# Optimization experiments

Hardware: AMD Instinct MI355X
Metric: run time of the kernel (lower is better)

The kernel has to match this reference:

```python
import jax, jax.numpy as jnp
import numpy as np

B, S, D = 8, 2048, 768
SCALE = jnp.sqrt(jnp.float32(D))


def setup_inputs() -> dict:
    key = jax.random.key(0)
    ks = jax.random.split(key, 9)
    sd = 1.0 / np.sqrt(D)
    return {
        "x": jax.random.normal(ks[0], (B, S, D), jnp.float32),
        "Wq": jax.random.normal(ks[1], (D, D), jnp.float32) * sd,
        "bq": jax.random.normal(ks[2], (D,), jnp.float32) * sd,
        "Wk": jax.random.normal(ks[3], (D, D), jnp.float32) * sd,
        "bk": jax.random.normal(ks[4], (D,), jnp.float32) * sd,
        "Wv": jax.random.normal(ks[5], (D, D), jnp.float32) * sd,
        "bv": jax.random.normal(ks[6], (D,), jnp.float32) * sd,
        "Wp": jax.random.normal(ks[7], (D, D), jnp.float32) * sd,
        "bp": jax.random.normal(ks[8], (D,), jnp.float32) * sd,
    }


def reference(x, Wq, bq, Wk, bk, Wv, bv, Wp, bp):
    # Linear layers: y = x @ W^T + b (torch nn.Linear convention)
    Q = jnp.einsum("bsd,ed->bse", x, Wq) + bq
    K = jnp.einsum("bsd,ed->bse", x, Wk) + bk
    V = jnp.einsum("bsd,ed->bse", x, Wv) + bv
    # Full attention matrix (no head split in original module)
    alpha = jnp.einsum("bqd,bkd->bqk", Q, K) / SCALE  # [B,S,S]
    alpha = jax.nn.softmax(alpha, axis=-1)
    # dropout is identity in eval mode
    out = jnp.einsum("bqk,bkd->bqd", alpha, V)
    out = jnp.einsum("bsd,ed->bse", out, Wp) + bp
    return out
```

## Files before the change

kernel.cpp:

```cpp
#include <hip/hip_runtime.h>
#include <stdint.h>


typedef __attribute__((ext_vector_type(8))) short short8;
typedef __attribute__((ext_vector_type(4))) float f32x4;

typedef const __attribute__((address_space(1))) void gvoid_t;
typedef __attribute__((address_space(3))) void lvoid_t;

__device__ __forceinline__ float b2f(unsigned short u) {
  union { unsigned int u; float f; } v;
  v.u = ((unsigned int)u) << 16;
  return v.f;
}
__device__ __forceinline__ unsigned short f2b(float f) {
  union { float f; unsigned int u; } v; v.f = f;
  unsigned int u = v.u;
  return (unsigned short)((u + 0x7fffu + ((u >> 16) & 1u)) >> 16);
}

struct Cvt9 {
  const void* s[9];
  unsigned short* d[9];
  long long n8[9];
  long long total8;
};

__global__ __launch_bounds__(256) void convert_inputs(Cvt9 C) {
  long long g = (long long)blockIdx.x * 256 + threadIdx.x;
  if (g >= C.total8) return;
  int s = 0;
  long long off = g;
  while (off >= C.n8[s]) { off -= C.n8[s]; ++s; }
  const float* sf = (const float*)C.s[s] + off * 8;
  unsigned short* dp = C.d[s] + off * 8;
  float4 a = ((const float4*)sf)[0];
  float4 b = ((const float4*)sf)[1];
  uint4 o;
  o.x = (unsigned int)f2b(a.x) | ((unsigned int)f2b(a.y) << 16);
  o.y = (unsigned int)f2b(a.z) | ((unsigned int)f2b(a.w) << 16);
  o.z = (unsigned int)f2b(b.x) | ((unsigned int)f2b(b.y) << 16);
  o.w = (unsigned int)f2b(b.z) | ((unsigned int)f2b(b.w) << 16);
  *(uint4*)dp = o;
}

__device__ __forceinline__ void gemm128(
    const unsigned short* __restrict__ Ag,
    const unsigned short* __restrict__ Bg,
    const int lda, const int ldb, const int NT,
    unsigned short* lds, f32x4 (&acc)[4][4])
{
  const int t    = threadIdx.x;
  const int w    = t >> 6;
  const int lane = t & 63;
  const int lo   = lane & 15;
  const int quad = lane >> 4;
  const int wr   = w >> 1;
  const int wc   = w & 1;
  const int srow = t >> 2;
  const int ssw  = ((t & 3) ^ (srow & 3)) << 3;

  const unsigned lbase = (unsigned)(uintptr_t)(void*)lds;
  const unsigned rsw   = (unsigned)((quad ^ (lo & 3)) << 4);
  const unsigned aAr   = lbase + (unsigned)(wr * 64 + lo) * 64 + rsw;
  const unsigned aBr   = lbase + 8192u + (unsigned)(wc * 64 + lo) * 64 + rsw;

#define STG(kt, buf) {                                                              \
  const unsigned short* a0_ = Ag + (size_t)(srow)      * lda + (kt) * 32 + ssw;     \
  const unsigned short* a1_ = Ag + (size_t)(64 + srow) * lda + (kt) * 32 + ssw;     \
  const unsigned short* b0_ = Bg + (size_t)(srow)      * ldb + (kt) * 32 + ssw;     \
  const unsigned short* b1_ = Bg + (size_t)(64 + srow) * ldb + (kt) * 32 + ssw;     \
  unsigned short* d_ = lds + (buf) * 8192 + t * 8;                                  \
  __builtin_amdgcn_global_load_lds((gvoid_t*)a0_, (lvoid_t*)(d_),        16, 0, 0); \
  __builtin_amdgcn_global_load_lds((gvoid_t*)a1_, (lvoid_t*)(d_ + 2048), 16, 0, 0); \
  __builtin_amdgcn_global_load_lds((gvoid_t*)b0_, (lvoid_t*)(d_ + 4096), 16, 0, 0); \
  __builtin_amdgcn_global_load_lds((gvoid_t*)b1_, (lvoid_t*)(d_ + 6144), 16, 0, 0); }
#define DSR(d, a, IMM) asm volatile("ds_read_b128 %0, %1 offset:" #IMM : "=v"(d) : "v"(a))
#define LGK(n) { asm volatile("s_waitcnt lgkmcnt(" #n ")" ::: "memory"); \
                 __builtin_amdgcn_sched_barrier(0); }
#define GRP(g) { _Pragma("unroll") for (int mi = 0; mi < 4; ++mi)             \
    acc[mi][g] = __builtin_amdgcn_mfma_f32_16x16x32_bf16(                     \
        af[mi], bf[g], acc[mi][g], 0, 0, 0); }

  STG(0, 0);
  __syncthreads();

  for (int kt = 0; kt < NT; ++kt) {
    const int buf = kt & 1;
    if (kt + 1 < NT) STG(kt + 1, buf ^ 1);

    const unsigned bo = (unsigned)(buf * 16384);
    short8 af[4], bf[4];
    const unsigned aA = aAr + bo, aB = aBr + bo;
    DSR(af[0], aA, 0); DSR(af[1], aA, 1024); DSR(af[2], aA, 2048); DSR(af[3], aA, 3072);
    DSR(bf[0], aB, 0); DSR(bf[1], aB, 1024); DSR(bf[2], aB, 2048); DSR(bf[3], aB, 3072);

    __builtin_amdgcn_s_setprio(1);
    LGK(3); GRP(0);
    LGK(2); GRP(1);
    LGK(1); GRP(2);
    LGK(0); GRP(3);
    __builtin_amdgcn_s_setprio(0);

    __syncthreads();
  }
#undef STG
#undef DSR
#undef LGK
#undef GRP
}

template<int MODE>
__device__ __forceinline__ void epi_bf16(
    unsigned short* Ls, f32x4 (&acc)[4][4],
    const unsigned short* bias_n0, const float* rlbase, float scale,
    unsigned short* Cg, int ldc, float* rlout)
{
  const int t = threadIdx.x, w = t >> 6, lane = t & 63;
  const int lo = lane & 15, quad = lane >> 4, wr = w >> 1, wc = w & 1;
#pragma unroll
  for (int h = 0; h < 2; ++h) {
    __syncthreads();
    if (wr == h) {
      float bvv[4];
      if (MODE == 0) {
#pragma unroll
        for (int ni = 0; ni < 4; ++ni) bvv[ni] = b2f(bias_n0[wc * 64 + ni * 16 + lo]);
      }
#pragma unroll
      for (int mi = 0; mi < 4; ++mi) {
        const int r0 = mi * 16 + quad * 4;
        float rv[4];
        if (MODE == 3) {
#pragma unroll
          for (int r = 0; r < 4; ++r) rv[r] = __builtin_amdgcn_rcpf(rlbase[h * 64 + r0 + r]);
        }
#pragma unroll
        for (int ni = 0; ni < 4; ++ni) {
          const int col = wc * 64 + ni * 16 + lo;
#pragma unroll
          for (int r = 0; r < 4; ++r) {
            float v = acc[mi][ni][r];
            if (MODE == 0)      v += bvv[ni];
            else if (MODE == 2) v = __expf(fminf(v * scale, 30.f));
            else if (MODE == 3) v *= rv[r];
            Ls[(r0 + r) * 136 + col] = f2b(v);
          }
        }
      }
    }
    __syncthreads();
#pragma unroll
    for (int j = 0; j < 4; ++j) {
      const int u = j * 256 + t, row = u >> 4, c16 = (u & 15) * 8;
      *(uint4*)(Cg + (size_t)(h * 64 + row) * ldc + c16) = *(const uint4*)(Ls + row * 136 + c16);
    }
    if (MODE == 2) {
      const int row = t >> 2, seg = t & 3;
      const unsigned short* lr = Ls + row * 136 + seg * 32;
      float s = 0.f;
#pragma unroll
      for (int q4 = 0; q4 < 4; ++q4) {
        uint4 v = *(const uint4*)(lr + q4 * 8);
        unsigned int uu[4] = {v.x, v.y, v.z, v.w};
#pragma unroll
        for (int c = 0; c < 4; ++c)
          s += b2f((unsigned short)(uu[c] & 0xffffu)) + b2f((unsigned short)(uu[c] >> 16));
      }
      s += __shfl_xor(s, 1);
      s += __shfl_xor(s, 2);
      if (seg == 0) atomicAdd(rlout + h * 64 + row, s);
    }
  }
}

__global__ __launch_bounds__(256, 4) void qkv_k(
    const unsigned short* __restrict__ xb,
    const unsigned short* __restrict__ Wq, const unsigned short* __restrict__ bq,
    const unsigned short* __restrict__ Wk, const unsigned short* __restrict__ bk,
    const unsigned short* __restrict__ Wv, const unsigned short* __restrict__ bv,
    unsigned short* __restrict__ qb, unsigned short* __restrict__ kb,
    unsigned short* __restrict__ vt)
{
  __shared__ unsigned short smem[16384];
  const int sel = blockIdx.y / 6;
  const int n0  = (blockIdx.y % 6) * 128;
  const int m0  = blockIdx.x * 128;

  const unsigned short* W;
  const unsigned short* bi;
  if (sel == 0)      { W = Wq; bi = bq; }
  else if (sel == 1) { W = Wk; bi = bk; }
  else               { W = Wv; bi = bv; }

  f32x4 acc[4][4] = {};
  gemm128(xb + (size_t)m0 * 768, W + (size_t)n0 * 768, 768, 768, 24, smem, acc);

  if (sel < 2) {
    unsigned short* dst = (sel == 0 ? qb : kb) + (size_t)m0 * 768 + n0;
    epi_bf16<0>(smem, acc, bi + n0, nullptr, 0.f, dst, 768, nullptr);
    return;
  }

  const int t = threadIdx.x, w = t >> 6, lane = t & 63;
  const int lo = lane & 15, quad = lane >> 4, wr = w >> 1, wc = w & 1;
  const int bb2 = m0 >> 11, sin = m0 & 2047;
  unsigned short* Ls = smem;
#pragma unroll
  for (int ec = 0; ec < 2; ++ec) {
    __syncthreads();
    if (wc == ec) {
#pragma unroll
      for (int ni = 0; ni < 4; ++ni) {
        const int el = ni * 16 + lo;
        const float bvv = b2f(bi[n0 + ec * 64 + el]);
#pragma unroll
        for (int mi = 0; mi < 4; ++mi) {
          const int srow2 = wr * 64 + mi * 16 + quad * 4;
          ushort4 pk;
          pk.x = f2b(acc[mi][ni][0] + bvv);
          pk.y = f2b(acc[mi][ni][1] + bvv);
          pk.z = f2b(acc[mi][ni][2] + bvv);
          pk.w = f2b(acc[mi][ni][3] + bvv);
          *(ushort4*)(Ls + el * 136 + srow2) = pk;
        }
      }
    }
    __syncthreads();
    unsigned short* Vb = vt + (size_t)bb2 * 1572864 + (size_t)(n0 + ec * 64) * 2048 + sin;
#pragma unroll
    for (int j = 0; j < 4; ++j) {
      const int u = j * 256 + t, e = u >> 4, s16 = (u & 15) * 8;
      *(uint4*)(Vb + (size_t)e * 2048 + s16) = *(const uint4*)(Ls + e * 136 + s16);
    }
  }
}

__global__ __launch_bounds__(256, 4) void score_k(
    const unsigned short* __restrict__ Q, const unsigned short* __restrict__ Kb,
    unsigned short* __restrict__ E, float* __restrict__ rl, float scale)
{
  __shared__ unsigned short smem[16384];
  const int m0 = blockIdx.x * 128, n0 = blockIdx.y * 128, bz = blockIdx.z;

  f32x4 acc[4][4] = {};
  gemm128(Q + (size_t)bz * 1572864 + (size_t)m0 * 768,
          Kb + (size_t)bz * 1572864 + (size_t)n0 * 768, 768, 768, 24, smem, acc);

  unsigned short* Eg = E + (size_t)bz * 4194304 + (size_t)m0 * 2048 + n0;
  epi_bf16<2>(smem, acc, nullptr, nullptr, scale, Eg, 2048, rl + bz * 2048 + m0);
}

__global__ __launch_bounds__(256, 4) void pv_k(
    const unsigned short* __restrict__ E, const unsigned short* __restrict__ Vt,
    const float* __restrict__ rl, unsigned short* __restrict__ attn)
{
  __shared__ unsigned short smem[16384];
  const int m0 = blockIdx.x * 128, n0 = blockIdx.y * 128, bz = blockIdx.z;

  f32x4 acc[4][4] = {};
  gemm128(E + (size_t)bz * 4194304 + (size_t)m0 * 2048,
          Vt + (size_t)bz * 1572864 + (size_t)n0 * 2048, 2048, 2048, 64, smem, acc);

  const float* rlb = rl + bz * 2048 + m0;
  unsigned short* Cg = attn + (size_t)bz * 1572864 + (size_t)m0 * 768 + n0;
  epi_bf16<3>(smem, acc, nullptr, rlb, 0.f, Cg, 768, nullptr);
}

__global__ __launch_bounds__(256, 4) void out_k(
    const unsigned short* __restrict__ attn,
    const unsigned short* __restrict__ Wp, const unsigned short* __restrict__ bp,
    float* __restrict__ Of)
{
  __shared__ unsigned short smem[16384];
  const int m0 = blockIdx.x * 128, n0 = blockIdx.y * 128;

  f32x4 acc[4][4] = {};
  gemm128(attn + (size_t)m0 * 768, Wp + (size_t)n0 * 768, 768, 768, 24, smem, acc);

  const int t = threadIdx.x, w = t >> 6, lane = t & 63;
  const int lo = lane & 15, quad = lane >> 4, wr = w >> 1, wc = w & 1;
  float* Lf = (float*)smem;
#pragma unroll
  for (int p = 0; p < 4; ++p) {
    __syncthreads();
    if (wr == (p >> 1)) {
#pragma unroll
      for (int mm = 0; mm < 2; ++mm) {
        const int mi = (p & 1) * 2 + mm;
        const int lr0 = mm * 16 + quad * 4;
#pragma unroll
        for (int ni = 0; ni < 4; ++ni) {
          const int col = wc * 64 + ni * 16 + lo;
          const float bvv = b2f(bp[n0 + col]);
#pragma unroll
          for (int r = 0; r < 4; ++r)
            Lf[(lr0 + r) * 132 + col] = acc[mi][ni][r] + bvv;
        }
      }
    }
    __syncthreads();
#pragma unroll
    for (int j = 0; j < 4; ++j) {
      const int u = j * 256 + t, row = u >> 5, c4 = (u & 31) * 4;
      *(float4*)(Of + (size_t)(m0 + p * 32 + row) * 768 + n0 + c4) =
          *(const float4*)(Lf + row * 132 + c4);
    }
  }
}

extern "C" void kernel_launch(void* const* d_in, const int* in_sizes, int n_in,
                              void* d_out, int out_size, void* d_ws, size_t ws_size,
                              hipStream_t stream) {
  (void)in_sizes; (void)n_in; (void)out_size; (void)ws_size;

  char* ws = (char*)d_ws;
  float* rl    = (float*)(ws + 4096);
  unsigned short* wcv = (unsigned short*)(ws + ((size_t)1 << 20));
  unsigned short* qb  = (unsigned short*)(ws + ((size_t)8  << 20));
  unsigned short* kb  = (unsigned short*)(ws + ((size_t)32 << 20));
  unsigned short* vt  = (unsigned short*)(ws + ((size_t)56 << 20));
  unsigned short* eb  = (unsigned short*)(ws + ((size_t)80 << 20));
  unsigned short* xb  = eb;
  unsigned short* attn = qb;

  unsigned short* wqb = wcv;
  unsigned short* bqb = wcv + 589824;
  unsigned short* wkb = wcv + 590592;
  unsigned short* bkb = wcv + 1180416;
  unsigned short* wvb = wcv + 1181184;
  unsigned short* bvb = wcv + 1771008;
  unsigned short* wpb = wcv + 1771776;
  unsigned short* bpb = wcv + 2361600;

  const float inv_scale = 0.036084391824351615f;

  Cvt9 cv;
  cv.s[0] = d_in[0]; cv.d[0] = xb;  cv.n8[0] = 12582912 / 8;
  cv.s[1] = d_in[1]; cv.d[1] = wqb; cv.n8[1] = 589824 / 8;
  cv.s[2] = d_in[2]; cv.d[2] = bqb; cv.n8[2] = 768 / 8;
  cv.s[3] = d_in[3]; cv.d[3] = wkb; cv.n8[3] = 589824 / 8;
  cv.s[4] = d_in[4]; cv.d[4] = bkb; cv.n8[4] = 768 / 8;
  cv.s[5] = d_in[5]; cv.d[5] = wvb; cv.n8[5] = 589824 / 8;
  cv.s[6] = d_in[6]; cv.d[6] = bvb; cv.n8[6] = 768 / 8;
  cv.s[7] = d_in[7]; cv.d[7] = wpb; cv.n8[7] = 589824 / 8;
  cv.s[8] = d_in[8]; cv.d[8] = bpb; cv.n8[8] = 768 / 8;
  cv.total8 = (12582912 + 4 * (589824 + 768)) / 8;
  convert_inputs<<<(unsigned)((cv.total8 + 255) / 256), dim3(256), 0, stream>>>(cv);

  hipMemsetAsync(rl, 0, 16384 * sizeof(float), stream);

  qkv_k<<<dim3(128, 18, 1), dim3(256), 0, stream>>>(xb, wqb, bqb, wkb, bkb, wvb, bvb, qb, kb, vt);

  score_k<<<dim3(16, 16, 8), dim3(256), 0, stream>>>(qb, kb, eb, rl, inv_scale);

  pv_k<<<dim3(16, 6, 8), dim3(256), 0, stream>>>(eb, vt, rl, attn);

  out_k<<<dim3(128, 6, 1), dim3(256), 0, stream>>>(attn, wpb, bpb, (float*)d_out);
}
```

Measured before the change: 352.1 us.

## Grow GEMM tiles to 256x128 with 512-thread blocks across all kernels

The GEMM helper now computes a 256x128 output tile with 8 waves per block instead of 128x128 with 4 waves. The B tile staged in shared memory is shared by twice as many rows, cutting global loads of the B operand per output element. LDS swizzles, epilogues, the V-transpose staging and the launch grids are adjusted to match. The cost is fewer blocks per launch (for example 512 score blocks instead of 1024), more shared memory per block, and possible occupancy limits under launch_bounds(512,4).

```diff
diff --git a/kernel.cpp b/kernel.cpp
--- a/kernel.cpp
+++ b/kernel.cpp
@@ -44,7 +44,7 @@
   *(uint4*)dp = o;
 }
 
-__device__ __forceinline__ void gemm128(
+__device__ __forceinline__ void gemm256(
     const unsigned short* __restrict__ Ag,
     const unsigned short* __restrict__ Bg,
     const int lda, const int ldb, const int NT,
@@ -58,23 +58,21 @@
   const int wr   = w >> 1;
   const int wc   = w & 1;
   const int srow = t >> 2;
-  const int ssw  = ((t & 3) ^ (srow & 3)) << 3;
+  const int ssw  = ((t & 3) ^ ((t >> 3) & 3)) << 3;
 
   const unsigned lbase = (unsigned)(uintptr_t)(void*)lds;
-  const unsigned rsw   = (unsigned)((quad ^ (lo & 3)) << 4);
+  const unsigned rsw   = (unsigned)((quad ^ ((lo >> 1) & 3)) << 4);
   const unsigned aAr   = lbase + (unsigned)(wr * 64 + lo) * 64 + rsw;
-  const unsigned aBr   = lbase + 8192u + (unsigned)(wc * 64 + lo) * 64 + rsw;
+  const unsigned aBr   = lbase + 16384u + (unsigned)(wc * 64 + lo) * 64 + rsw;
 
 #define STG(kt, buf) {                                                              \
-  const unsigned short* a0_ = Ag + (size_t)(srow)      * lda + (kt) * 32 + ssw;     \
-  const unsigned short* a1_ = Ag + (size_t)(64 + srow) * lda + (kt) * 32 + ssw;     \
-  const unsigned short* b0_ = Bg + (size_t)(srow)      * ldb + (kt) * 32 + ssw;     \
-  const unsigned short* b1_ = Bg + (size_t)(64 + srow) * ldb + (kt) * 32 + ssw;     \
-  unsigned short* d_ = lds + (buf) * 8192 + t * 8;                                  \
+  const unsigned short* a0_ = Ag + (size_t)(srow)       * lda + (kt) * 32 + ssw;    \
+  const unsigned short* a1_ = Ag + (size_t)(128 + srow) * lda + (kt) * 32 + ssw;    \
+  const unsigned short* b0_ = Bg + (size_t)(srow)       * ldb + (kt) * 32 + ssw;    \
+  unsigned short* d_ = lds + (buf) * 12288 + t * 8;                                 \
   __builtin_amdgcn_global_load_lds((gvoid_t*)a0_, (lvoid_t*)(d_),        16, 0, 0); \
-  __builtin_amdgcn_global_load_lds((gvoid_t*)a1_, (lvoid_t*)(d_ + 2048), 16, 0, 0); \
-  __builtin_amdgcn_global_load_lds((gvoid_t*)b0_, (lvoid_t*)(d_ + 4096), 16, 0, 0); \
-  __builtin_amdgcn_global_load_lds((gvoid_t*)b1_, (lvoid_t*)(d_ + 6144), 16, 0, 0); }
+  __builtin_amdgcn_global_load_lds((gvoid_t*)a1_, (lvoid_t*)(d_ + 4096), 16, 0, 0); \
+  __builtin_amdgcn_global_load_lds((gvoid_t*)b0_, (lvoid_t*)(d_ + 8192), 16, 0, 0); }
 #define DSR(d, a, IMM) asm volatile("ds_read_b128 %0, %1 offset:" #IMM : "=v"(d) : "v"(a))
 #define LGK(n) { asm volatile("s_waitcnt lgkmcnt(" #n ")" ::: "memory"); \
                  __builtin_amdgcn_sched_barrier(0); }
@@ -89,7 +87,7 @@
     const int buf = kt & 1;
     if (kt + 1 < NT) STG(kt + 1, buf ^ 1);
 
-    const unsigned bo = (unsigned)(buf * 16384);
+    const unsigned bo = (unsigned)(buf * 24576);
     short8 af[4], bf[4];
     const unsigned aA = aAr + bo, aB = aBr + bo;
     DSR(af[0], aA, 0); DSR(af[1], aA, 1024); DSR(af[2], aA, 2048); DSR(af[3], aA, 3072);
@@ -121,7 +119,7 @@
 #pragma unroll
   for (int h = 0; h < 2; ++h) {
     __syncthreads();
-    if (wr == h) {
+    if ((wr >> 1) == h) {
       float bvv[4];
       if (MODE == 0) {
 #pragma unroll
@@ -129,11 +127,11 @@
       }
 #pragma unroll
       for (int mi = 0; mi < 4; ++mi) {
-        const int r0 = mi * 16 + quad * 4;
+        const int r0 = (wr & 1) * 64 + mi * 16 + quad * 4;
         float rv[4];
         if (MODE == 3) {
 #pragma unroll
-          for (int r = 0; r < 4; ++r) rv[r] = __builtin_amdgcn_rcpf(rlbase[h * 64 + r0 + r]);
+          for (int r = 0; r < 4; ++r) rv[r] = __builtin_amdgcn_rcpf(rlbase[h * 128 + r0 + r]);
         }
 #pragma unroll
         for (int ni = 0; ni < 4; ++ni) {
@@ -152,8 +150,8 @@
     __syncthreads();
 #pragma unroll
     for (int j = 0; j < 4; ++j) {
-      const int u = j * 256 + t, row = u >> 4, c16 = (u & 15) * 8;
-      *(uint4*)(Cg + (size_t)(h * 64 + row) * ldc + c16) = *(const uint4*)(Ls + row * 136 + c16);
+      const int u = j * 512 + t, row = u >> 4, c16 = (u & 15) * 8;
+      *(uint4*)(Cg + (size_t)(h * 128 + row) * ldc + c16) = *(const uint4*)(Ls + row * 136 + c16);
     }
     if (MODE == 2) {
       const int row = t >> 2, seg = t & 3;
@@ -169,12 +167,12 @@
       }
       s += __shfl_xor(s, 1);
       s += __shfl_xor(s, 2);
-      if (seg == 0) atomicAdd(rlout + h * 64 + row, s);
-    }
-  }
-}
-
-__global__ __launch_bounds__(256, 4) void qkv_k(
+      if (seg == 0) atomicAdd(rlout + h * 128 + row, s);
+    }
+  }
+}
+
+__global__ __launch_bounds__(512, 4) void qkv_k(
     const unsigned short* __restrict__ xb,
     const unsigned short* __restrict__ Wq, const unsigned short* __restrict__ bq,
     const unsigned short* __restrict__ Wk, const unsigned short* __restrict__ bk,
@@ -182,10 +180,10 @@
     unsigned short* __restrict__ qb, unsigned short* __restrict__ kb,
     unsigned short* __restrict__ vt)
 {
-  __shared__ unsigned short smem[16384];
+  __shared__ unsigned short smem[24576];
   const int sel = blockIdx.y / 6;
   const int n0  = (blockIdx.y % 6) * 128;
-  const int m0  = blockIdx.x * 128;
+  const int m0  = blockIdx.x * 256;
 
   const unsigned short* W;
   const unsigned short* bi;
@@ -194,7 +192,7 @@
   else               { W = Wv; bi = bv; }
 
   f32x4 acc[4][4] = {};
-  gemm128(xb + (size_t)m0 * 768, W + (size_t)n0 * 768, 768, 768, 24, smem, acc);
+  gemm256(xb + (size_t)m0 * 768, W + (size_t)n0 * 768, 768, 768, 24, smem, acc);
 
   if (sel < 2) {
     unsigned short* dst = (sel == 0 ? qb : kb) + (size_t)m0 * 768 + n0;
@@ -216,13 +214,13 @@
         const float bvv = b2f(bi[n0 + ec * 64 + el]);
 #pragma unroll
         for (int mi = 0; mi < 4; ++mi) {
-          const int srow2 = wr * 64 + mi * 16 + quad * 4;
+          const int sl = wr * 64 + mi * 16 + quad * 4;
           ushort4 pk;
           pk.x = f2b(acc[mi][ni][0] + bvv);
           pk.y = f2b(acc[mi][ni][1] + bvv);
           pk.z = f2b(acc[mi][ni][2] + bvv);
           pk.w = f2b(acc[mi][ni][3] + bvv);
-          *(ushort4*)(Ls + el * 136 + srow2) = pk;
+          *(ushort4*)(Ls + el * 264 + sl) = pk;
         }
       }
     }
@@ -230,36 +228,36 @@
     unsigned short* Vb = vt + (size_t)bb2 * 1572864 + (size_t)(n0 + ec * 64) * 2048 + sin;
 #pragma unroll
     for (int j = 0; j < 4; ++j) {
-      const int u = j * 256 + t, e = u >> 4, s16 = (u & 15) * 8;
-      *(uint4*)(Vb + (size_t)e * 2048 + s16) = *(const uint4*)(Ls + e * 136 + s16);
-    }
-  }
-}
-
-__global__ __launch_bounds__(256, 4) void score_k(
+      const int u = j * 512 + t, e = u >> 5, s16 = (u & 31) * 8;
+      *(uint4*)(Vb + (size_t)e * 2048 + s16) = *(const uint4*)(Ls + e * 264 + s16);
+    }
+  }
+}
+
+__global__ __launch_bounds__(512, 4) void score_k(
     const unsigned short* __restrict__ Q, const unsigned short* __restrict__ Kb,
     unsigned short* __restrict__ E, float* __restrict__ rl, float scale)
 {
-  __shared__ unsigned short smem[16384];
-  const int m0 = blockIdx.x * 128, n0 = blockIdx.y * 128, bz = blockIdx.z;
+  __shared__ unsigned short smem[24576];
+  const int m0 = blockIdx.x * 256, n0 = blockIdx.y * 128, bz = blockIdx.z;
 
   f32x4 acc[4][4] = {};
-  gemm128(Q + (size_t)bz * 1572864 + (size_t)m0 * 768,
+  gemm256(Q + (size_t)bz * 1572864 + (size_t)m0 * 768,
           Kb + (size_t)bz * 1572864 + (size_t)n0 * 768, 768, 768, 24, smem, acc);
 
   unsigned short* Eg = E + (size_t)bz * 4194304 + (size_t)m0 * 2048 + n0;
   epi_bf16<2>(smem, acc, nullptr, nullptr, scale, Eg, 2048, rl + bz * 2048 + m0);
 }
 
-__global__ __launch_bounds__(256, 4) void pv_k(
+__global__ __launch_bounds__(512, 4) void pv_k(
     const unsigned short* __restrict__ E, const unsigned short* __restrict__ Vt,
     const float* __restrict__ rl, unsigned short* __restrict__ attn)
 {
-  __shared__ unsigned short smem[16384];
-  const int m0 = blockIdx.x * 128, n0 = blockIdx.y * 128, bz = blockIdx.z;
+  __shared__ unsigned short smem[24576];
+  const int m0 = blockIdx.x * 256, n0 = blockIdx.y * 128, bz = blockIdx.z;
 
   f32x4 acc[4][4] = {};
-  gemm128(E + (size_t)bz * 4194304 + (size_t)m0 * 2048,
+  gemm256(E + (size_t)bz * 4194304 + (size_t)m0 * 2048,
           Vt + (size_t)bz * 1572864 + (size_t)n0 * 2048, 2048, 2048, 64, smem, acc);
 
   const float* rlb = rl + bz * 2048 + m0;
@@ -267,16 +265,16 @@
   epi_bf16<3>(smem, acc, nullptr, rlb, 0.f, Cg, 768, nullptr);
 }
 
-__global__ __launch_bounds__(256, 4) void out_k(
+__global__ __launch_bounds__(512, 4) void out_k(
     const unsigned short* __restrict__ attn,
     const unsigned short* __restrict__ Wp, const unsigned short* __restrict__ bp,
     float* __restrict__ Of)
 {
-  __shared__ unsigned short smem[16384];
-  const int m0 = blockIdx.x * 128, n0 = blockIdx.y * 128;
+  __shared__ unsigned short smem[24576];
+  const int m0 = blockIdx.x * 256, n0 = blockIdx.y * 128;
 
   f32x4 acc[4][4] = {};
-  gemm128(attn + (size_t)m0 * 768, Wp + (size_t)n0 * 768, 768, 768, 24, smem, acc);
+  gemm256(attn + (size_t)m0 * 768, Wp + (size_t)n0 * 768, 768, 768, 24, smem, acc);
 
   const int t = threadIdx.x, w = t >> 6, lane = t & 63;
   const int lo = lane & 15, quad = lane >> 4, wr = w >> 1, wc = w & 1;
@@ -284,27 +282,30 @@
 #pragma unroll
   for (int p = 0; p < 4; ++p) {
     __syncthreads();
-    if (wr == (p >> 1)) {
-#pragma unroll
-      for (int mm = 0; mm < 2; ++mm) {
-        const int mi = (p & 1) * 2 + mm;
-        const int lr0 = mm * 16 + quad * 4;
+    if (wr == p) {
+#pragma unroll
+      for (int mi = 0; mi < 4; ++mi) {
+        const int r0 = mi * 16 + quad * 4;
 #pragma unroll
         for (int ni = 0; ni < 4; ++ni) {
           const int col = wc * 64 + ni * 16 + lo;
           const float bvv = b2f(bp[n0 + col]);
 #pragma unroll
           for (int r = 0; r < 4; ++r)
-            Lf[(lr0 + r) * 132 + col] = acc[mi][ni][r] + bvv;
+            Lf[(r0 + r) * 132 + col] = acc[mi][ni][r] + bvv;
         }
       }
     }
     __syncthreads();
 #pragma unroll
-    for (int j = 0; j < 4; ++j) {
-      const int u = j * 256 + t, row = u >> 5, c4 = (u & 31) * 4;
-      *(float4*)(Of + (size_t)(m0 + p * 32 + row) * 768 + n0 + c4) =
-          *(const float4*)(Lf + row * 132 + c4);
+    for (int j = 0; j < 2; ++j) {
+      const int u = j * 512 + t, row = u >> 4, c4 = (u & 15) * 8;
+      const float* src = Lf + row * 132 + c4;
+      float4 v0 = *(const float4*)(src);
+      float4 v1 = *(const float4*)(src + 4);
+      float* dst = Of + (size_t)(m0 + p * 64 + row) * 768 + n0 + c4;
+      *(float4*)(dst) = v0;
+      *(float4*)(dst + 4) = v1;
     }
   }
 }
@@ -350,11 +351,11 @@
 
   hipMemsetAsync(rl, 0, 16384 * sizeof(float), stream);
 
-  qkv_k<<<dim3(128, 18, 1), dim3(256), 0, stream>>>(xb, wqb, bqb, wkb, bkb, wvb, bvb, qb, kb, vt);
-
-  score_k<<<dim3(16, 16, 8), dim3(256), 0, stream>>>(qb, kb, eb, rl, inv_scale);
-
-  pv_k<<<dim3(16, 6, 8), dim3(256), 0, stream>>>(eb, vt, rl, attn);
-
-  out_k<<<dim3(128, 6, 1), dim3(256), 0, stream>>>(attn, wpb, bpb, (float*)d_out);
-}
+  qkv_k<<<dim3(64, 18, 1), dim3(512), 0, stream>>>(xb, wqb, bqb, wkb, bkb, wvb, bvb, qb, kb, vt);
+
+  score_k<<<dim3(8, 16, 8), dim3(512), 0, stream>>>(qb, kb, eb, rl, inv_scale);
+
+  pv_k<<<dim3(8, 6, 8), dim3(512), 0, stream>>>(eb, vt, rl, attn);
+
+  out_k<<<dim3(64, 6, 1), dim3(512), 0, stream>>>(attn, wpb, bpb, (float*)d_out);
+}
```

New measurement: 342.2 us. 1.03x faster.
